# Optimization experiments

Measured on AMD Instinct MI355X. Metric: run time of the kernel, lower is better.

Reference implementation:

```python
import jax, jax.numpy as jnp
import numpy as np

B, S, L = 256, 20, 512
SKILL_DIM, HIDDEN = 128, 768
VOCAB = 2001


def setup_inputs() -> dict:
    key = jax.random.key(0)
    k1, k2, k3, k4 = jax.random.split(key, 4)
    skills = jax.random.randint(k1, (B, S), 0, VOCAB)
    desc = jax.random.normal(k2, (B, L, HIDDEN), dtype=jnp.float32)
    embs = jax.random.normal(k3, (VOCAB, SKILL_DIM), dtype=jnp.float32)
    W = jax.random.normal(k4, (SKILL_DIM, HIDDEN), dtype=jnp.float32)
    return {"skills": skills, "desc": desc, "embs": embs, "W": W}


def reference(skills, desc, embs, W):
    # skills: [B,S] int, desc: [B,L,H], embs: [V,D], W: [D,H]
    se = embs[skills]                                  # [B,S,D] embedding lookup
    q = jnp.einsum('bsd,dh->bsh', se, W)               # [B,S,H]
    scores = jnp.einsum('bsh,blh->bsl', q, desc)       # [B,S,L] unscaled QK^T
    attn = jax.nn.softmax(scores, axis=2)              # softmax over desc tokens
    out = jnp.einsum('bsl,blh->bsh', attn, desc)       # [B,S,H]
    cat = jnp.concatenate([se, out], axis=2)           # [B,S,D+H]
    return cat.reshape(cat.shape[0], -1)               # [B, S*(D+H)]
```

## Files before the change

### kernel.cpp

```cpp
#include <hip/hip_runtime.h>
#include <cstddef>
#include <cstdint>

#define NB 256
#define NS 20
#define NL 512
#define ND 128
#define NH 768
#define ROWE (NS*(ND+NH))

typedef __attribute__((ext_vector_type(4))) float  f32x4;
typedef __attribute__((ext_vector_type(8))) short  bf16x8;
typedef __attribute__((ext_vector_type(4))) unsigned short ushort4v;

#define MFMA16 __builtin_amdgcn_mfma_f32_16x16x32_bf16

__device__ __forceinline__ unsigned short bf16_rne(float v){
    unsigned u = __builtin_bit_cast(unsigned, v);
    u = (u + 0x7fffu + ((u>>16)&1u)) >> 16;
    return (unsigned short)u;
}
__device__ __forceinline__ float bf16f(unsigned short h){
    unsigned u = ((unsigned)h)<<16;
    return __builtin_bit_cast(float, u);
}
__device__ __forceinline__ void bar_lds(){
    asm volatile("s_waitcnt lgkmcnt(0)" ::: "memory");
    __builtin_amdgcn_s_barrier();
}

extern "C" __global__ __launch_bounds__(256)
void k1_q(const int* __restrict__ skills, const float* __restrict__ embs,
          const float* __restrict__ W,
          unsigned short* __restrict__ qhi, unsigned short* __restrict__ qlo,
          float* __restrict__ out)
{
    __shared__ float se[NS*ND];
    __shared__ int   sk[NS];
    const int b = blockIdx.x, t = threadIdx.x;
    if (t < NS) sk[t] = skills[b*NS + t];
    __syncthreads();
    for (int idx = t; idx < NS*ND; idx += 256) {
        const int s = idx >> 7, d = idx & (ND-1);
        const float v = embs[(size_t)sk[s]*ND + d];
        se[idx] = v;
        out[(size_t)b*ROWE + (size_t)s*(ND+NH) + d] = v;
    }
    __syncthreads();

    const int w = t >> 6, lane = t & 63;
    float acc[5][12];
    #pragma unroll
    for (int i = 0; i < 5; ++i)
        #pragma unroll
        for (int c = 0; c < 12; ++c) acc[i][c] = 0.f;

    const float* Wl = W + lane;
    for (int d4 = 0; d4 < ND/4; ++d4) {
        f32x4 sv[5];
        #pragma unroll
        for (int i = 0; i < 5; ++i)
            sv[i] = *(const f32x4*)&se[(5*w + i)*ND + 4*d4];
        #pragma unroll
        for (int r = 0; r < 4; ++r) {
            const float* wr = Wl + (size_t)(4*d4 + r)*NH;
            float wv[12];
            #pragma unroll
            for (int c = 0; c < 12; ++c) wv[c] = wr[64*c];
            #pragma unroll
            for (int i = 0; i < 5; ++i) {
                const float s_ = sv[i][r];
                #pragma unroll
                for (int c = 0; c < 12; ++c) acc[i][c] += s_*wv[c];
            }
        }
    }
    #pragma unroll
    for (int i = 0; i < 5; ++i)
        #pragma unroll
        for (int c = 0; c < 12; ++c) {
            const size_t idx = ((size_t)b*NS + 5*w + i)*NH + lane + 64*c;
            const float v = acc[i][c];
            const unsigned short hh = bf16_rne(v);
            qhi[idx] = hh;
            qlo[idx] = bf16_rne(v - bf16f(hh));
        }
}

#define DTFP  772
#define CPR   193

extern "C" __global__ __launch_bounds__(512)
void k2f(const unsigned short* __restrict__ qhi,
         const unsigned short* __restrict__ qlo,
         const float* __restrict__ desc,
         float* __restrict__ Opart, float* __restrict__ ms)
{
    __shared__ __align__(16) float dtf[12544];
    __shared__ __align__(16) f32x4 scr[3][2][64];
    __shared__ __align__(16) float p_lds2[16][24];
    __shared__ float f_lds[2][16];

    const int b = blockIdx.x, lh = blockIdx.y, t = threadIdx.x;
    const int w = t >> 6, L = t & 63;
    const int st = w & 1, kq = w >> 1;
    const int g = L >> 4, r16 = L & 15;
    const int slot = t % 96, sq = t / 96;

    const float* dsrc = desc + ((size_t)b*NL + (size_t)lh*256)*NH;
    const int s_in = 16*st + r16;
    const size_t qrow = ((size_t)b*NS + (s_in < NS ? s_in : NS-1))*(size_t)NH;

    bf16x8 qhreg[6], qlreg[6];
    #pragma unroll
    for (int kb = 0; kb < 6; ++kb) {
        const int k0 = 192*kq + 32*kb + 8*g;
        qhreg[kb] = *(const bf16x8*)&qhi[qrow + k0];
        qlreg[kb] = *(const bf16x8*)&qlo[qrow + k0];
    }

    f32x4 acc4[4][2];
    #pragma unroll
    for (int j = 0; j < 4; ++j) {
        acc4[j][0] = (f32x4){0.f,0.f,0.f,0.f};
        acc4[j][1] = (f32x4){0.f,0.f,0.f,0.f};
    }
    float m_run = -1e30f, sum_run = 0.f;

    auto issue_dma = [&](const float* tsrc){
        #pragma unroll
        for (int i = 0; i < 6; ++i) {
            const int ch = 8*i + w;
            const unsigned s = (unsigned)(ch*64 + L);
            unsigned row = (s*5434u) >> 20;
            unsigned col = s - row*CPR;
            if (row > 15u) row = 15u;
            if (col > 191u) col = 191u;
            const float* gsrc = tsrc + (size_t)row*NH + 4u*col;
            __builtin_amdgcn_global_load_lds(gsrc, &dtf[ch*256], 16, 0, 0);
        }
        if (w == 0) {
            const unsigned s = (unsigned)(48*64 + L);
            unsigned row = (s*5434u) >> 20;
            unsigned col = s - row*CPR;
            if (row > 15u) row = 15u;
            if (col > 191u) col = 191u;
            const float* gsrc = tsrc + (size_t)row*NH + 4u*col;
            __builtin_amdgcn_global_load_lds(gsrc, &dtf[48*256], 16, 0, 0);
        }
    };

    issue_dma(dsrc);
    asm volatile("s_waitcnt vmcnt(0)" ::: "memory");
    bar_lds();

    #pragma unroll 1
    for (int tt = 0; tt < 16; ++tt) {
        f32x4 Se = (f32x4){0.f,0.f,0.f,0.f};
        #pragma unroll
        for (int kb = 0; kb < 6; ++kb) {
            const int k0 = 192*kq + 32*kb;
            const f32x4 A0 = *(const f32x4*)&dtf[r16*DTFP + k0 + 8*g];
            const f32x4 A1 = *(const f32x4*)&dtf[r16*DTFP + k0 + 8*g + 4];
            ushort4v h0, h1, l0, l1;
            #pragma unroll
            for (int e = 0; e < 4; ++e) {
                const float x0 = A0[e], x1 = A1[e];
                const unsigned short hh0 = bf16_rne(x0);
                const unsigned short hh1 = bf16_rne(x1);
                h0[e] = hh0;  h1[e] = hh1;
                l0[e] = (unsigned short)(__builtin_bit_cast(unsigned, x0 - bf16f(hh0)) >> 16);
                l1[e] = (unsigned short)(__builtin_bit_cast(unsigned, x1 - bf16f(hh1)) >> 16);
            }
            const bf16x8 Ah = __builtin_bit_cast(bf16x8,
                __builtin_shufflevector(h0, h1, 0,1,2,3,4,5,6,7));
            const bf16x8 Al = __builtin_bit_cast(bf16x8,
                __builtin_shufflevector(l0, l1, 0,1,2,3,4,5,6,7));
            Se = MFMA16(Ah, qhreg[kb], Se, 0,0,0);
            Se = MFMA16(Al, qhreg[kb], Se, 0,0,0);
            Se = MFMA16(Ah, qlreg[kb], Se, 0,0,0);
        }
        if (kq > 0) scr[kq-1][st][L] = Se;
        bar_lds();

        if (kq == 0) {
            Se += scr[0][st][L];
            Se += scr[1][st][L];
            Se += scr[2][st][L];
            float pm = fmaxf(fmaxf(Se[0],Se[1]), fmaxf(Se[2],Se[3]));
            pm = fmaxf(pm, __shfl_xor(pm, 16));
            pm = fmaxf(pm, __shfl_xor(pm, 32));
            const float mnew = fmaxf(m_run, pm);
            const float fsc  = __expf(m_run - mnew);
            float pe[4];
            #pragma unroll
            for (int r = 0; r < 4; ++r) pe[r] = __expf(Se[r] - mnew);
            float ts = (pe[0]+pe[1]) + (pe[2]+pe[3]);
            ts += __shfl_xor(ts, 16);
            ts += __shfl_xor(ts, 32);
            sum_run = sum_run*fsc + ts;
            m_run = mnew;
            if (s_in < NS) {
                #pragma unroll
                for (int r = 0; r < 4; ++r)
                    p_lds2[4*g + r][s_in] = pe[r];
            }
            if (L < 16) f_lds[st][L] = fsc;
        }
        bar_lds();

        if (sq < 5) {
            #pragma unroll
            for (int j = 0; j < 4; ++j) {
                const int s = 4*sq + j;
                const float f = f_lds[s>>4][s&15];
                acc4[j][0] *= f;  acc4[j][1] *= f;
            }
            #pragma unroll
            for (int l = 0; l < 16; ++l) {
                const f32x4 d0 = *(const f32x4*)&dtf[l*DTFP + 4*slot];
                const f32x4 d1 = *(const f32x4*)&dtf[l*DTFP + 384 + 4*slot];
                const f32x4 pv = *(const f32x4*)&p_lds2[l][4*sq];
                acc4[0][0] += pv[0] * d0;  acc4[0][1] += pv[0] * d1;
                acc4[1][0] += pv[1] * d0;  acc4[1][1] += pv[1] * d1;
                acc4[2][0] += pv[2] * d0;  acc4[2][1] += pv[2] * d1;
                acc4[3][0] += pv[3] * d0;  acc4[3][1] += pv[3] * d1;
            }
        }
        bar_lds();

        if (tt < 15) {
            issue_dma(dsrc + (size_t)(tt+1)*16*NH);
            asm volatile("s_waitcnt vmcnt(0)" ::: "memory");
            bar_lds();
        }
    }

    bar_lds();
    if (kq == 0 && L < 16) f_lds[st][L] = 1.0f / sum_run;
    bar_lds();
    if (sq < 5) {
        #pragma unroll
        for (int j = 0; j < 4; ++j) {
            const int s = 4*sq + j;
            const float inv = f_lds[s>>4][s&15];
            float* Ob = Opart + ((size_t)(b*2 + lh)*NS + s)*NH;
            f32x4 o0 = acc4[j][0], o1 = acc4[j][1];
            o0 *= inv;  o1 *= inv;
            *(f32x4*)&Ob[4*slot]       = o0;
            *(f32x4*)&Ob[384 + 4*slot] = o1;
        }
    }
    if (kq == 0 && L < 16) {
        const int s2 = 16*st + L;
        if (s2 < NS) {
            ms[((size_t)(b*2 + lh)*NS + s2)*2 + 0] = m_run;
            ms[((size_t)(b*2 + lh)*NS + s2)*2 + 1] = sum_run;
        }
    }
}

extern "C" __global__ __launch_bounds__(256)
void k3_fin(const float* __restrict__ Opart, const float* __restrict__ ms,
            float* __restrict__ out)
{
    __shared__ float c0s[NS], c1s[NS];
    const int b = blockIdx.x, t = threadIdx.x;
    if (t < NS) {
        const float m0 = ms[((size_t)(b*2 + 0)*NS + t)*2 + 0];
        const float s0 = ms[((size_t)(b*2 + 0)*NS + t)*2 + 1];
        const float m1 = ms[((size_t)(b*2 + 1)*NS + t)*2 + 0];
        const float s1 = ms[((size_t)(b*2 + 1)*NS + t)*2 + 1];
        const float m  = fmaxf(m0, m1);
        const float w0 = __expf(m0 - m)*s0, w1 = __expf(m1 - m)*s1;
        const float inv = 1.0f / (w0 + w1);
        c0s[t] = w0*inv;
        c1s[t] = w1*inv;
    }
    __syncthreads();
    const float* O0 = Opart + (size_t)(b*2 + 0)*NS*NH;
    const float* O1 = Opart + (size_t)(b*2 + 1)*NS*NH;
    #pragma unroll 1
    for (int i4 = t; i4 < NS*NH/4; i4 += 256) {
        const int idx = 4*i4;
        const int s = idx / NH, h = idx - s*NH;
        const f32x4 a = *(const f32x4*)&O0[idx];
        const f32x4 c = *(const f32x4*)&O1[idx];
        const float c0 = c0s[s], c1 = c1s[s];
        f32x4 o;
        o[0] = c0*a[0] + c1*c[0]; o[1] = c0*a[1] + c1*c[1];
        o[2] = c0*a[2] + c1*c[2]; o[3] = c0*a[3] + c1*c[3];
        *(f32x4*)&out[(size_t)b*ROWE + (size_t)s*(ND+NH) + ND + h] = o;
    }
}

extern "C" void kernel_launch(void* const* d_in, const int* in_sizes, int n_in,
                              void* d_out, int out_size, void* d_ws, size_t ws_size,
                              hipStream_t stream)
{
    const int*   skills = (const int*)  d_in[0];
    const float* desc   = (const float*)d_in[1];
    const float* embs   = (const float*)d_in[2];
    const float* W      = (const float*)d_in[3];
    float* out = (float*)d_out;

    unsigned short* qhi = (unsigned short*)d_ws;
    unsigned short* qlo = qhi + (size_t)NB*NS*NH;
    float* Opart = (float*)(qlo + (size_t)NB*NS*NH);
    float* ms    = Opart + (size_t)NB*2*NS*NH;

    k1_q  <<<NB,          256, 0, stream>>>(skills, embs, W, qhi, qlo, out);
    k2f   <<<dim3(NB, 2), 512, 0, stream>>>(qhi, qlo, desc, Opart, ms);
    k3_fin<<<NB,          256, 0, stream>>>(Opart, ms, out);
}
```

Measured before the change: 208.0 us.

## Read desc tiles directly from global memory instead of staging through LDS

```diff
diff --git a/kernel.cpp b/kernel.cpp
--- a/kernel.cpp
+++ b/kernel.cpp
@@ -1,4 +1,5 @@
 #include <hip/hip_runtime.h>
+#include <hip/hip_bf16.h>
 #include <cstddef>
 #include <cstdint>
 
@@ -87,16 +88,12 @@
         }
 }
 
-#define DTFP  772
-#define CPR   193
-
 extern "C" __global__ __launch_bounds__(512)
 void k2f(const unsigned short* __restrict__ qhi,
          const unsigned short* __restrict__ qlo,
          const float* __restrict__ desc,
          float* __restrict__ Opart, float* __restrict__ ms)
 {
-    __shared__ __align__(16) float dtf[12544];
     __shared__ __align__(16) f32x4 scr[3][2][64];
     __shared__ __align__(16) float p_lds2[16][24];
     __shared__ float f_lds[2][16];
@@ -127,41 +124,17 @@
     }
     float m_run = -1e30f, sum_run = 0.f;
 
-    auto issue_dma = [&](const float* tsrc){
-        #pragma unroll
-        for (int i = 0; i < 6; ++i) {
-            const int ch = 8*i + w;
-            const unsigned s = (unsigned)(ch*64 + L);
-            unsigned row = (s*5434u) >> 20;
-            unsigned col = s - row*CPR;
-            if (row > 15u) row = 15u;
-            if (col > 191u) col = 191u;
-            const float* gsrc = tsrc + (size_t)row*NH + 4u*col;
-            __builtin_amdgcn_global_load_lds(gsrc, &dtf[ch*256], 16, 0, 0);
-        }
-        if (w == 0) {
-            const unsigned s = (unsigned)(48*64 + L);
-            unsigned row = (s*5434u) >> 20;
-            unsigned col = s - row*CPR;
-            if (row > 15u) row = 15u;
-            if (col > 191u) col = 191u;
-            const float* gsrc = tsrc + (size_t)row*NH + 4u*col;
-            __builtin_amdgcn_global_load_lds(gsrc, &dtf[48*256], 16, 0, 0);
-        }
-    };
-
-    issue_dma(dsrc);
-    asm volatile("s_waitcnt vmcnt(0)" ::: "memory");
-    bar_lds();
-
     #pragma unroll 1
     for (int tt = 0; tt < 16; ++tt) {
+        const float* tsrc = dsrc + (size_t)tt*16*NH;
+
         f32x4 Se = (f32x4){0.f,0.f,0.f,0.f};
         #pragma unroll
         for (int kb = 0; kb < 6; ++kb) {
             const int k0 = 192*kq + 32*kb;
-            const f32x4 A0 = *(const f32x4*)&dtf[r16*DTFP + k0 + 8*g];
-            const f32x4 A1 = *(const f32x4*)&dtf[r16*DTFP + k0 + 8*g + 4];
+            const float* arow = tsrc + (size_t)r16*NH + k0 + 8*g;
+            const f32x4 A0 = *(const f32x4*)&arow[0];
+            const f32x4 A1 = *(const f32x4*)&arow[4];
             ushort4v h0, h1, l0, l1;
             #pragma unroll
             for (int e = 0; e < 4; ++e) {
@@ -169,8 +142,8 @@
                 const unsigned short hh0 = bf16_rne(x0);
                 const unsigned short hh1 = bf16_rne(x1);
                 h0[e] = hh0;  h1[e] = hh1;
-                l0[e] = (unsigned short)(__builtin_bit_cast(unsigned, x0 - bf16f(hh0)) >> 16);
-                l1[e] = (unsigned short)(__builtin_bit_cast(unsigned, x1 - bf16f(hh1)) >> 16);
+                l0[e] = bf16_rne(x0 - bf16f(hh0));
+                l1[e] = bf16_rne(x1 - bf16f(hh1));
             }
             const bf16x8 Ah = __builtin_bit_cast(bf16x8,
                 __builtin_shufflevector(h0, h1, 0,1,2,3,4,5,6,7));
@@ -216,23 +189,17 @@
                 const float f = f_lds[s>>4][s&15];
                 acc4[j][0] *= f;  acc4[j][1] *= f;
             }
-            #pragma unroll
+            #pragma unroll 4
             for (int l = 0; l < 16; ++l) {
-                const f32x4 d0 = *(const f32x4*)&dtf[l*DTFP + 4*slot];
-                const f32x4 d1 = *(const f32x4*)&dtf[l*DTFP + 384 + 4*slot];
+                const float* drow = tsrc + (size_t)l*NH;
+                const f32x4 d0 = *(const f32x4*)&drow[4*slot];
+                const f32x4 d1 = *(const f32x4*)&drow[384 + 4*slot];
                 const f32x4 pv = *(const f32x4*)&p_lds2[l][4*sq];
                 acc4[0][0] += pv[0] * d0;  acc4[0][1] += pv[0] * d1;
                 acc4[1][0] += pv[1] * d0;  acc4[1][1] += pv[1] * d1;
                 acc4[2][0] += pv[2] * d0;  acc4[2][1] += pv[2] * d1;
                 acc4[3][0] += pv[3] * d0;  acc4[3][1] += pv[3] * d1;
             }
-        }
-        bar_lds();
-
-        if (tt < 15) {
-            issue_dma(dsrc + (size_t)(tt+1)*16*NH);
-            asm volatile("s_waitcnt vmcnt(0)" ::: "memory");
-            bar_lds();
         }
     }
 
```

Result: slower. 289.1 us (+39.0%).

## Compute PV product with bf16 MFMA and overlap next tile DMA with compute

Applied to the files above, without the earlier changes.

```diff
diff --git a/kernel.cpp b/kernel.cpp
--- a/kernel.cpp
+++ b/kernel.cpp
@@ -11,9 +11,19 @@
 
 typedef __attribute__((ext_vector_type(4))) float  f32x4;
 typedef __attribute__((ext_vector_type(8))) short  bf16x8;
+typedef __attribute__((ext_vector_type(4))) short  short4v;
 typedef __attribute__((ext_vector_type(4))) unsigned short ushort4v;
+typedef __attribute__((ext_vector_type(8))) unsigned short ushort8v;
 
 #define MFMA16 __builtin_amdgcn_mfma_f32_16x16x32_bf16
+
+#if defined(__has_builtin)
+#  if __has_builtin(__builtin_amdgcn_mfma_f32_16x16x16bf16_1k)
+#    define MFMA_PV(a,b,c) __builtin_amdgcn_mfma_f32_16x16x16bf16_1k(a,b,c,0,0,0)
+#  elif __has_builtin(__builtin_amdgcn_mfma_f32_16x16x16_bf16)
+#    define MFMA_PV(a,b,c) __builtin_amdgcn_mfma_f32_16x16x16_bf16(a,b,c,0,0,0)
+#  endif
+#endif
 
 __device__ __forceinline__ unsigned short bf16_rne(float v){
     unsigned u = __builtin_bit_cast(unsigned, v);
@@ -97,15 +107,14 @@
          float* __restrict__ Opart, float* __restrict__ ms)
 {
     __shared__ __align__(16) float dtf[12544];
-    __shared__ __align__(16) f32x4 scr[3][2][64];
-    __shared__ __align__(16) float p_lds2[16][24];
+    __shared__ __align__(16) unsigned short vt[768*16];
+    __shared__ __align__(16) unsigned short p_lds2[2][16][20];
     __shared__ float f_lds[2][16];
 
     const int b = blockIdx.x, lh = blockIdx.y, t = threadIdx.x;
     const int w = t >> 6, L = t & 63;
     const int st = w & 1, kq = w >> 1;
     const int g = L >> 4, r16 = L & 15;
-    const int slot = t % 96, sq = t / 96;
 
     const float* dsrc = desc + ((size_t)b*NL + (size_t)lh*256)*NH;
     const int s_in = 16*st + r16;
@@ -119,12 +128,9 @@
         qlreg[kb] = *(const bf16x8*)&qlo[qrow + k0];
     }
 
-    f32x4 acc4[4][2];
+    f32x4 acc[12];
     #pragma unroll
-    for (int j = 0; j < 4; ++j) {
-        acc4[j][0] = (f32x4){0.f,0.f,0.f,0.f};
-        acc4[j][1] = (f32x4){0.f,0.f,0.f,0.f};
-    }
+    for (int i = 0; i < 12; ++i) acc[i] = (f32x4){0.f,0.f,0.f,0.f};
     float m_run = -1e30f, sum_run = 0.f;
 
     auto issue_dma = [&](const float* tsrc){
@@ -151,17 +157,19 @@
     };
 
     issue_dma(dsrc);
-    asm volatile("s_waitcnt vmcnt(0)" ::: "memory");
-    bar_lds();
 
     #pragma unroll 1
     for (int tt = 0; tt < 16; ++tt) {
+        asm volatile("s_waitcnt vmcnt(0)" ::: "memory");
+        bar_lds();
+
         f32x4 Se = (f32x4){0.f,0.f,0.f,0.f};
         #pragma unroll
         for (int kb = 0; kb < 6; ++kb) {
             const int k0 = 192*kq + 32*kb;
-            const f32x4 A0 = *(const f32x4*)&dtf[r16*DTFP + k0 + 8*g];
-            const f32x4 A1 = *(const f32x4*)&dtf[r16*DTFP + k0 + 8*g + 4];
+            const float* arow = &dtf[r16*DTFP + k0 + 8*g];
+            const f32x4 A0 = *(const f32x4*)&arow[0];
+            const f32x4 A1 = *(const f32x4*)&arow[4];
             ushort4v h0, h1, l0, l1;
             #pragma unroll
             for (int e = 0; e < 4; ++e) {
@@ -169,8 +177,8 @@
                 const unsigned short hh0 = bf16_rne(x0);
                 const unsigned short hh1 = bf16_rne(x1);
                 h0[e] = hh0;  h1[e] = hh1;
-                l0[e] = (unsigned short)(__builtin_bit_cast(unsigned, x0 - bf16f(hh0)) >> 16);
-                l1[e] = (unsigned short)(__builtin_bit_cast(unsigned, x1 - bf16f(hh1)) >> 16);
+                l0[e] = bf16_rne(x0 - bf16f(hh0));
+                l1[e] = bf16_rne(x1 - bf16f(hh1));
             }
             const bf16x8 Ah = __builtin_bit_cast(bf16x8,
                 __builtin_shufflevector(h0, h1, 0,1,2,3,4,5,6,7));
@@ -180,13 +188,33 @@
             Se = MFMA16(Al, qhreg[kb], Se, 0,0,0);
             Se = MFMA16(Ah, qlreg[kb], Se, 0,0,0);
         }
-        if (kq > 0) scr[kq-1][st][L] = Se;
+        {
+            f32x4* scr = (f32x4*)vt;
+            if (kq > 0) scr[((kq-1)*2 + st)*64 + L] = Se;
+        }
         bar_lds();
 
+        if (tt < 15) issue_dma(dsrc + (size_t)(tt+1)*16*NH);
+
+        ushort8v v0bf[3];
+        {
+            const float* tsrc = dsrc + (size_t)tt*16*NH;
+            #pragma unroll
+            for (int rep = 0; rep < 3; ++rep) {
+                const int u = 512*rep + t;
+                const int h = u >> 1, half = u & 1;
+                const float* gs = tsrc + (size_t)(8*half)*NH + h;
+                #pragma unroll
+                for (int e = 0; e < 8; ++e)
+                    v0bf[rep][e] = bf16_rne(gs[(size_t)e*NH]);
+            }
+        }
+
         if (kq == 0) {
-            Se += scr[0][st][L];
-            Se += scr[1][st][L];
-            Se += scr[2][st][L];
+            const f32x4* scr = (const f32x4*)vt;
+            Se += scr[(0*2 + st)*64 + L];
+            Se += scr[(1*2 + st)*64 + L];
+            Se += scr[(2*2 + st)*64 + L];
             float pm = fmaxf(fmaxf(Se[0],Se[1]), fmaxf(Se[2],Se[3]));
             pm = fmaxf(pm, __shfl_xor(pm, 16));
             pm = fmaxf(pm, __shfl_xor(pm, 32));
@@ -203,52 +231,75 @@
             if (s_in < NS) {
                 #pragma unroll
                 for (int r = 0; r < 4; ++r)
-                    p_lds2[4*g + r][s_in] = pe[r];
+                    p_lds2[st][r16][4*g + r] = bf16_rne(pe[r]);
             }
             if (L < 16) f_lds[st][L] = fsc;
         }
         bar_lds();
 
-        if (sq < 5) {
-            #pragma unroll
-            for (int j = 0; j < 4; ++j) {
-                const int s = 4*sq + j;
-                const float f = f_lds[s>>4][s&15];
-                acc4[j][0] *= f;  acc4[j][1] *= f;
-            }
-            #pragma unroll
-            for (int l = 0; l < 16; ++l) {
-                const f32x4 d0 = *(const f32x4*)&dtf[l*DTFP + 4*slot];
-                const f32x4 d1 = *(const f32x4*)&dtf[l*DTFP + 384 + 4*slot];
-                const f32x4 pv = *(const f32x4*)&p_lds2[l][4*sq];
-                acc4[0][0] += pv[0] * d0;  acc4[0][1] += pv[0] * d1;
-                acc4[1][0] += pv[1] * d0;  acc4[1][1] += pv[1] * d1;
-                acc4[2][0] += pv[2] * d0;  acc4[2][1] += pv[2] * d1;
-                acc4[3][0] += pv[3] * d0;  acc4[3][1] += pv[3] * d1;
-            }
+        #pragma unroll
+        for (int rep = 0; rep < 3; ++rep) {
+            const int u = 512*rep + t;
+            const int h = u >> 1, half = u & 1;
+            *(ushort8v*)&vt[h*16 + 8*half] = v0bf[rep];
         }
         bar_lds();
 
-        if (tt < 15) {
-            issue_dma(dsrc + (size_t)(tt+1)*16*NH);
-            asm volatile("s_waitcnt vmcnt(0)" ::: "memory");
-            bar_lds();
-        }
+        const float f0 = f_lds[0][r16], f1 = f_lds[1][r16];
+        #pragma unroll
+        for (int i = 0; i < 12; ++i) {
+            const float ff = (i & 1) ? f1 : f0;
+            acc[i][0]*=ff; acc[i][1]*=ff; acc[i][2]*=ff; acc[i][3]*=ff;
+        }
+#ifdef MFMA_PV
+        const short4v pb0 = *(const short4v*)&p_lds2[0][r16][4*g];
+        const short4v pb1 = *(const short4v*)&p_lds2[1][r16][4*g];
+        #pragma unroll
+        for (int hti = 0; hti < 6; ++hti) {
+            const int hrow = 16*(w + 8*hti) + r16;
+            const short4v av = *(const short4v*)&vt[hrow*16 + 4*g];
+            acc[2*hti+0] = MFMA_PV(av, pb0, acc[2*hti+0]);
+            acc[2*hti+1] = MFMA_PV(av, pb1, acc[2*hti+1]);
+        }
+#else
+        #pragma unroll
+        for (int hti = 0; hti < 6; ++hti) {
+            const int hb = 16*(w + 8*hti) + 4*g;
+            #pragma unroll
+            for (int st2 = 0; st2 < 2; ++st2) {
+                f32x4 a = acc[2*hti+st2];
+                #pragma unroll
+                for (int l = 0; l < 16; ++l) {
+                    const float pl = bf16f(p_lds2[st2][r16][l]);
+                    #pragma unroll
+                    for (int j = 0; j < 4; ++j)
+                        a[j] += pl * bf16f(vt[(hb + j)*16 + l]);
+                }
+                acc[2*hti+st2] = a;
+            }
+        }
+#endif
     }
 
     bar_lds();
     if (kq == 0 && L < 16) f_lds[st][L] = 1.0f / sum_run;
     bar_lds();
-    if (sq < 5) {
-        #pragma unroll
-        for (int j = 0; j < 4; ++j) {
-            const int s = 4*sq + j;
-            const float inv = f_lds[s>>4][s&15];
-            float* Ob = Opart + ((size_t)(b*2 + lh)*NS + s)*NH;
-            f32x4 o0 = acc4[j][0], o1 = acc4[j][1];
-            o0 *= inv;  o1 *= inv;
-            *(f32x4*)&Ob[4*slot]       = o0;
-            *(f32x4*)&Ob[384 + 4*slot] = o1;
+    {
+        const float i0 = f_lds[0][r16], i1 = f_lds[1][r16];
+        float* Ob = Opart + (size_t)(b*2 + lh)*NS*NH;
+        #pragma unroll
+        for (int hti = 0; hti < 6; ++hti) {
+            const int ht = w + 8*hti;
+            #pragma unroll
+            for (int st2 = 0; st2 < 2; ++st2) {
+                const int s = 16*st2 + r16;
+                if (s < NS) {
+                    const float inv = st2 ? i1 : i0;
+                    f32x4 o = acc[2*hti+st2];
+                    o[0]*=inv; o[1]*=inv; o[2]*=inv; o[3]*=inv;
+                    *(f32x4*)&Ob[(size_t)s*NH + 16*ht + 4*g] = o;
+                }
+            }
         }
     }
     if (kq == 0 && L < 16) {
```

Result: slower. 236.9 us (+13.9%).
